# Kernel optimization log

Measured on AMD Instinct MI355X. Metric: run time of the kernel, lower is better.

Reference implementation:

```python
import jax, jax.numpy as jnp
import numpy as np

NUM_HEADS = 16


def setup_inputs() -> dict:
    key = jax.random.key(0)
    ks = jax.random.split(key, 6)
    B, N, M, D = 4, 2048, 2048, 1024
    s = 1.0 / np.sqrt(D)
    return {
        "inputs": jax.random.normal(ks[0], (B, N, D), dtype=jnp.float32),
        "encoderOutputs": jax.random.normal(ks[1], (B, M, D), dtype=jnp.float32),
        "wq": jax.random.normal(ks[2], (D, D), dtype=jnp.float32) * s,
        "wk": jax.random.normal(ks[3], (D, D), dtype=jnp.float32) * s,
        "wv": jax.random.normal(ks[4], (D, D), dtype=jnp.float32) * s,
        "wo": jax.random.normal(ks[5], (D, D), dtype=jnp.float32) * s,
    }


def reference(inputs, encoderOutputs, wq, wk, wv, wo):
    B, N, D = inputs.shape
    M = encoderOutputs.shape[1]
    H = NUM_HEADS
    hd = D // H
    # Linear layers (no bias; torch Linear computes x @ W.T, weights here stored as [dOut,dIn])
    q = (inputs @ wq.T).reshape(B, N, H, hd).transpose(0, 2, 1, 3)        # [B,H,N,hd]
    k = (encoderOutputs @ wk.T).reshape(B, M, H, hd).transpose(0, 2, 1, 3)  # [B,H,M,hd]
    v = (encoderOutputs @ wv.T).reshape(B, M, H, hd).transpose(0, 2, 1, 3)  # [B,H,M,hd]
    scores = jnp.einsum('bhnd,bhmd->bhnm', q, k) / jnp.sqrt(jnp.float32(hd))
    attn = jax.nn.softmax(scores, axis=-1)  # dropout p=0.0 -> identity
    ctx = jnp.einsum('bhnm,bhmd->bhnd', attn, v)
    ctx = ctx.transpose(0, 2, 1, 3).reshape(B, N, D)
    return ctx @ wo.T
```

## Files before the change

kernel.cpp:

```cpp
#include <hip/hip_runtime.h>
#include <hip/hip_bf16.h>


typedef __attribute__((ext_vector_type(8))) short bf16x8;
typedef __attribute__((ext_vector_type(4))) float f32x4;
typedef __attribute__((ext_vector_type(16))) float f32x16;
typedef __attribute__((ext_vector_type(4))) unsigned short u16x4;
typedef __attribute__((ext_vector_type(4))) unsigned int u32x4;

#define SEQ 2048
#define H_ 16

static __device__ __forceinline__ unsigned short f2bf(float f) {
  unsigned int u = __float_as_uint(f);
  u += 0x7fffu + ((u >> 16) & 1u);
  return (unsigned short)(u >> 16);
}

static __device__ __forceinline__ void gload16(const void* g, void* l) {
  __builtin_amdgcn_global_load_lds((const __attribute__((address_space(1))) void*)g,
                                   (__attribute__((address_space(3))) void*)l, 16, 0, 0);
}

__global__ __launch_bounds__(256) void k_cvt_all(const float* __restrict__ x, const float* __restrict__ e,
    const float* __restrict__ wq, const float* __restrict__ wk,
    const float* __restrict__ wv, const float* __restrict__ wo,
    unsigned short* __restrict__ Xb, unsigned short* __restrict__ Eb,
    unsigned short* __restrict__ Wqb, unsigned short* __restrict__ Wkb,
    unsigned short* __restrict__ Wvb, unsigned short* __restrict__ Wob) {
  int i = blockIdx.x * 256 + threadIdx.x;
  const float* src; unsigned short* dst; int off;
  if (i < 2097152)      { src = x;  dst = Xb;  off = i; }
  else if (i < 4194304) { src = e;  dst = Eb;  off = i - 2097152; }
  else if (i < 4456448) { src = wq; dst = Wqb; off = i - 4194304; }
  else if (i < 4718592) { src = wk; dst = Wkb; off = i - 4456448; }
  else if (i < 4980736) { src = wv; dst = Wvb; off = i - 4718592; }
  else                  { src = wo; dst = Wob; off = i - 4980736; }
  float4 v = reinterpret_cast<const float4*>(src)[off];
  u16x4 o;
  o[0] = f2bf(v.x); o[1] = f2bf(v.y); o[2] = f2bf(v.z); o[3] = f2bf(v.w);
  *reinterpret_cast<u16x4*>(dst + (size_t)off * 4) = o;
}

template<typename EPI>
static __device__ __forceinline__ void gemm_core(const unsigned short* __restrict__ A,
                                                 const unsigned short* __restrict__ W,
                                                 int col0, int row0, EPI epi) {
  __shared__ __align__(16) unsigned short As[128 * 32];
  __shared__ __align__(16) unsigned short Bs[128 * 32];
  const int tid = threadIdx.x, lane = tid & 63, w = tid >> 6;
  const int wr = w >> 1, wc = w & 1;
  f32x4 acc[4][4];
  for (int i = 0; i < 4; ++i)
    for (int j = 0; j < 4; ++j)
      for (int e = 0; e < 4; ++e) acc[i][j][e] = 0.f;
  const unsigned short* Ag[2];
  const unsigned short* Wg[2];
  unsigned short* Al[2];
  unsigned short* Bl[2];
  for (int p = 0; p < 2; ++p) {
    int ci = p * 4 + w;
    int eo = ci * 512 + lane * 8;
    int r = eo >> 5, c = eo & 31;
    Ag[p] = A + (size_t)(row0 + r) * 1024 + c;
    Wg[p] = W + (size_t)(col0 + r) * 1024 + c;
    Al[p] = &As[ci * 512];
    Bl[p] = &Bs[ci * 512];
  }
  const int fr = lane & 15, ko = (lane >> 4) * 8;
  for (int k0 = 0; k0 < 1024; k0 += 32) {
    __syncthreads();
    for (int p = 0; p < 2; ++p) {
      gload16(Ag[p] + k0, Al[p]);
      gload16(Wg[p] + k0, Bl[p]);
    }
    __syncthreads();
    bf16x8 af[4], bfr[4];
    for (int mi = 0; mi < 4; ++mi)
      af[mi] = *(const bf16x8*)&As[(wr * 64 + mi * 16 + fr) * 32 + ko];
    for (int ni = 0; ni < 4; ++ni)
      bfr[ni] = *(const bf16x8*)&Bs[(wc * 64 + ni * 16 + fr) * 32 + ko];
    for (int mi = 0; mi < 4; ++mi)
      for (int ni = 0; ni < 4; ++ni)
        acc[mi][ni] = __builtin_amdgcn_mfma_f32_16x16x32_bf16(af[mi], bfr[ni], acc[mi][ni], 0, 0, 0);
  }
  for (int mi = 0; mi < 4; ++mi)
    for (int ni = 0; ni < 4; ++ni) {
      int r0 = row0 + wr * 64 + mi * 16 + (lane >> 4) * 4;
      int o = col0 + wc * 64 + ni * 16 + (lane & 15);
      epi(r0, o, acc[mi][ni]);
    }
}

__global__ __launch_bounds__(256) void k_gemm_qkv(const unsigned short* __restrict__ Xb,
                                                  const unsigned short* __restrict__ Eb,
                                                  const unsigned short* __restrict__ Wqb,
                                                  const unsigned short* __restrict__ Wkb,
                                                  const unsigned short* __restrict__ Wvb,
                                                  unsigned short* __restrict__ Qb,
                                                  unsigned short* __restrict__ Kb,
                                                  unsigned short* __restrict__ Vtg) {
  const int z = blockIdx.z;
  const int col0 = blockIdx.x * 128, row0 = blockIdx.y * 128;
  const unsigned short* A = (z == 0) ? Xb : Eb;
  const unsigned short* W = (z == 0) ? Wqb : (z == 1) ? Wkb : Wvb;
  if (z == 2) {
    gemm_core(A, W, col0, row0, [&](int r0, int o, f32x4 v) {
      int b = r0 >> 11, n0 = r0 & (SEQ - 1);
      int h = o >> 6, c = o & 63;
      u16x4 o4;
      for (int j = 0; j < 4; ++j) o4[j] = f2bf(v[j]);
      *(u16x4*)&Vtg[(((size_t)(b * H_ + h)) * 64 + c) * SEQ + n0] = o4;
    });
  } else {
    unsigned short* out = (z == 0) ? Qb : Kb;
    const float sc = (z == 0) ? 0.18033688f : 1.0f;
    gemm_core(A, W, col0, row0, [&](int r0, int o, f32x4 v) {
      int b = r0 >> 11, n0 = r0 & (SEQ - 1);
      int h = o >> 6, c = o & 63;
      for (int j = 0; j < 4; ++j)
        out[(((size_t)(b * H_ + h)) * SEQ + n0 + j) * 64 + c] = f2bf(v[j] * sc);
    });
  }
}

__global__ __launch_bounds__(256) void k_gemm_out(const unsigned short* __restrict__ A,
                                                  const unsigned short* __restrict__ W,
                                                  float* __restrict__ out) {
  const int col0 = blockIdx.x * 128, row0 = blockIdx.y * 128;
  gemm_core(A, W, col0, row0, [&](int r0, int o, f32x4 v) {
    for (int j = 0; j < 4; ++j)
      out[(size_t)(r0 + j) * 1024 + o] = v[j];
  });
}

static __device__ __forceinline__ int swzaddr(int row, int colb) {
  return row * 128 + (colb ^ ((row & 7) << 4));
}

__global__ __launch_bounds__(512) void k_attn(const unsigned short* __restrict__ Qh,
                                              const unsigned short* __restrict__ Kh,
                                              const unsigned short* __restrict__ Vtg,
                                              unsigned short* __restrict__ CTX) {
  __shared__ __align__(16) char lds[4 * 8192];
  const int tid = threadIdx.x, lane = tid & 63, w = tid >> 6;
  const int hi = lane >> 5, q = lane & 31;
  const int id = blockIdx.x;
  const int bh = (id & 7) * 8 + ((id >> 3) & 7);
  const int qt = id >> 6;
  const size_t kvbase = (size_t)bh * (SEQ * 64);
  const size_t qrow = (size_t)bh * SEQ + qt * 256 + w * 32 + q;
  bf16x8 qf[4];
#pragma unroll
  for (int c = 0; c < 4; ++c)
    qf[c] = *(const bf16x8*)&Qh[qrow * 64 + c * 16 + hi * 8];
  f32x16 oacc0, oacc1, oaccL, fzero;
#pragma unroll
  for (int r = 0; r < 16; ++r) { oacc0[r] = 0.f; oacc1[r] = 0.f; oaccL[r] = 0.f; fzero[r] = 0.f; }
  bf16x8 ones;
#pragma unroll
  for (int r = 0; r < 8; ++r) ones[r] = (short)0x3F80;

  const int sc = tid;
  const int srow = sc >> 3, spb = (sc & 7) << 4;
  const int sge = (spb ^ ((srow & 7) << 4)) >> 1;
  const size_t koff = (size_t)srow * 64 + sge;
  const size_t voff = (size_t)srow * SEQ + sge;
  const int ldso = sc * 16;

#define STAGE(T, BUFO)                                                        \
  {                                                                           \
    gload16(Kh + kvbase + (size_t)(T) * 4096 + koff, lds + (BUFO) + ldso);    \
    gload16(Vtg + kvbase + (size_t)(T) * 64 + voff, lds + (BUFO) + 8192 + ldso); \
  }

  STAGE(0, 0);

  for (int t = 0; t < 32; ++t) {
    __syncthreads();
    const int bo = (t & 1) * 16384;
    char* Kb = lds + bo;
    char* Vb = lds + bo + 8192;
    if (t + 1 < 32) STAGE(t + 1, ((t + 1) & 1) * 16384);

    f32x16 s0, s1;
    __builtin_amdgcn_s_setprio(1);
    {
      bf16x8 kf0 = *(const bf16x8*)(Kb + swzaddr(q, 0 * 32 + hi * 16));
      bf16x8 kf1 = *(const bf16x8*)(Kb + swzaddr(32 + q, 0 * 32 + hi * 16));
      s0 = __builtin_amdgcn_mfma_f32_32x32x16_bf16(kf0, qf[0], fzero, 0, 0, 0);
      s1 = __builtin_amdgcn_mfma_f32_32x32x16_bf16(kf1, qf[0], fzero, 0, 0, 0);
    }
#pragma unroll
    for (int c = 1; c < 4; ++c) {
      bf16x8 kf0 = *(const bf16x8*)(Kb + swzaddr(q, c * 32 + hi * 16));
      bf16x8 kf1 = *(const bf16x8*)(Kb + swzaddr(32 + q, c * 32 + hi * 16));
      s0 = __builtin_amdgcn_mfma_f32_32x32x16_bf16(kf0, qf[c], s0, 0, 0, 0);
      s1 = __builtin_amdgcn_mfma_f32_32x32x16_bf16(kf1, qf[c], s1, 0, 0, 0);
    }
    __builtin_amdgcn_s_setprio(0);

    bf16x8 pfrag[4];

#define SOFT_PACK(SREG, FA, FB)                                               \
    {                                                                         \
      float pa[16];                                                           \
      _Pragma("unroll")                                                       \
      for (int r = 0; r < 16; ++r) pa[r] = __builtin_amdgcn_exp2f(SREG[r]);   \
      unsigned pw[8];                                                         \
      _Pragma("unroll")                                                       \
      for (int i = 0; i < 8; ++i)                                             \
        asm("v_cvt_pk_bf16_f32 %0, %1, %2" : "=v"(pw[i])                      \
            : "v"(pa[2 * i]), "v"(pa[2 * i + 1]));                            \
      asm("v_permlane32_swap_b32 %0, %1" : "+v"(pw[0]), "+v"(pw[2]));         \
      asm("v_permlane32_swap_b32 %0, %1" : "+v"(pw[1]), "+v"(pw[3]));         \
      asm("v_permlane32_swap_b32 %0, %1" : "+v"(pw[4]), "+v"(pw[6]));         \
      asm("v_permlane32_swap_b32 %0, %1" : "+v"(pw[5]), "+v"(pw[7]));         \
      u32x4 fa = { pw[0], pw[1], pw[2], pw[3] };                              \
      u32x4 fb = { pw[4], pw[5], pw[6], pw[7] };                              \
      FA = __builtin_bit_cast(bf16x8, fa);                                    \
      FB = __builtin_bit_cast(bf16x8, fb);                                    \
    }

    SOFT_PACK(s0, pfrag[0], pfrag[1])
    SOFT_PACK(s1, pfrag[2], pfrag[3])
#undef SOFT_PACK

    __builtin_amdgcn_s_setprio(1);
#pragma unroll
    for (int kk = 0; kk < 4; ++kk) {
      bf16x8 vf0 = *(const bf16x8*)(Vb + swzaddr(q, kk * 32 + hi * 16));
      bf16x8 vf1 = *(const bf16x8*)(Vb + swzaddr(32 + q, kk * 32 + hi * 16));
      oacc0 = __builtin_amdgcn_mfma_f32_32x32x16_bf16(vf0, pfrag[kk], oacc0, 0, 0, 0);
      oacc1 = __builtin_amdgcn_mfma_f32_32x32x16_bf16(vf1, pfrag[kk], oacc1, 0, 0, 0);
      oaccL = __builtin_amdgcn_mfma_f32_32x32x16_bf16(ones, pfrag[kk], oaccL, 0, 0, 0);
    }
    __builtin_amdgcn_s_setprio(0);
  }
#undef STAGE

  const float inv = 1.0f / oaccL[0];
  const int b = bh >> 4, h = bh & 15;
  const size_t orow = ((size_t)b * SEQ + qt * 256 + w * 32 + q) * 1024 + h * 64;
#pragma unroll
  for (int g = 0; g < 4; ++g) {
    u16x4 o0, o1;
#pragma unroll
    for (int j = 0; j < 4; ++j) {
      o0[j] = f2bf(oacc0[g * 4 + j] * inv);
      o1[j] = f2bf(oacc1[g * 4 + j] * inv);
    }
    *(u16x4*)&CTX[orow + g * 8 + hi * 4] = o0;
    *(u16x4*)&CTX[orow + 32 + g * 8 + hi * 4] = o1;
  }
}

extern "C" void kernel_launch(void* const* d_in, const int* in_sizes, int n_in,
                              void* d_out, int out_size, void* d_ws, size_t ws_size,
                              hipStream_t stream) {
  const float* x  = (const float*)d_in[0];
  const float* e  = (const float*)d_in[1];
  const float* wq = (const float*)d_in[2];
  const float* wk = (const float*)d_in[3];
  const float* wv = (const float*)d_in[4];
  const float* wo = (const float*)d_in[5];
  unsigned short* Xb  = (unsigned short*)d_ws;
  unsigned short* Eb  = Xb + 8388608;
  unsigned short* Wqb = Eb + 8388608;
  unsigned short* Wkb = Wqb + 1048576;
  unsigned short* Wvb = Wkb + 1048576;
  unsigned short* Wob = Wvb + 1048576;
  unsigned short* Qb  = Wob + 1048576;
  unsigned short* Kb  = Qb + 8388608;
  unsigned short* Vtg = Kb + 8388608;
  unsigned short* Cb  = Vtg + 8388608;

  k_cvt_all<<<20480, 256, 0, stream>>>(x, e, wq, wk, wv, wo, Xb, Eb, Wqb, Wkb, Wvb, Wob);

  k_gemm_qkv<<<dim3(8, 64, 3), 256, 0, stream>>>(Xb, Eb, Wqb, Wkb, Wvb, Qb, Kb, Vtg);

  k_attn<<<512, 512, 0, stream>>>(Qb, Kb, Vtg, Cb);

  k_gemm_out<<<dim3(8, 64), 256, 0, stream>>>(Cb, Wob, (float*)d_out);
}
```

Before: 206.9 us.

## Fuse fp32-to-bf16 activation conversion into QKV GEMM tile loads

The separate conversion pass no longer writes bf16 copies of the inputs and encoder outputs. The QKV GEMM now loads fp32 activation tiles straight into LDS with an XOR swizzle and converts them to bf16 in registers with v_cvt_pk_bf16_f32 before the MFMAs. This removes a full read-write pass over the 32MB of activations and one extra round trip through memory. In exchange the GEMM A-tile traffic doubles (fp32 instead of bf16), the A LDS buffer grows, and conversion work is repeated by every column block that reuses the same A tile.

```diff
diff --git a/kernel.cpp b/kernel.cpp
--- a/kernel.cpp
+++ b/kernel.cpp
@@ -22,65 +22,113 @@
                                    (__attribute__((address_space(3))) void*)l, 16, 0, 0);
 }
 
-__global__ __launch_bounds__(256) void k_cvt_all(const float* __restrict__ x, const float* __restrict__ e,
-    const float* __restrict__ wq, const float* __restrict__ wk,
+__global__ __launch_bounds__(256) void k_cvt_w(const float* __restrict__ wq, const float* __restrict__ wk,
     const float* __restrict__ wv, const float* __restrict__ wo,
-    unsigned short* __restrict__ Xb, unsigned short* __restrict__ Eb,
     unsigned short* __restrict__ Wqb, unsigned short* __restrict__ Wkb,
     unsigned short* __restrict__ Wvb, unsigned short* __restrict__ Wob) {
   int i = blockIdx.x * 256 + threadIdx.x;
   const float* src; unsigned short* dst; int off;
-  if (i < 2097152)      { src = x;  dst = Xb;  off = i; }
-  else if (i < 4194304) { src = e;  dst = Eb;  off = i - 2097152; }
-  else if (i < 4456448) { src = wq; dst = Wqb; off = i - 4194304; }
-  else if (i < 4718592) { src = wk; dst = Wkb; off = i - 4456448; }
-  else if (i < 4980736) { src = wv; dst = Wvb; off = i - 4718592; }
-  else                  { src = wo; dst = Wob; off = i - 4980736; }
+  if (i < 262144)       { src = wq; dst = Wqb; off = i; }
+  else if (i < 524288)  { src = wk; dst = Wkb; off = i - 262144; }
+  else if (i < 786432)  { src = wv; dst = Wvb; off = i - 524288; }
+  else                  { src = wo; dst = Wob; off = i - 786432; }
   float4 v = reinterpret_cast<const float4*>(src)[off];
   u16x4 o;
   o[0] = f2bf(v.x); o[1] = f2bf(v.y); o[2] = f2bf(v.z); o[3] = f2bf(v.w);
   *reinterpret_cast<u16x4*>(dst + (size_t)off * 4) = o;
 }
 
-template<typename EPI>
-static __device__ __forceinline__ void gemm_core(const unsigned short* __restrict__ A,
+template<int F32A, typename EPI>
+static __device__ __forceinline__ void gemm_core(const void* __restrict__ Av,
                                                  const unsigned short* __restrict__ W,
                                                  int col0, int row0, EPI epi) {
-  __shared__ __align__(16) unsigned short As[128 * 32];
-  __shared__ __align__(16) unsigned short Bs[128 * 32];
+  constexpr int ABYTES = F32A ? 16384 : 8192;
+  __shared__ __align__(16) char AsB[ABYTES];
+  __shared__ __align__(16) unsigned short Ws[128 * 32];
   const int tid = threadIdx.x, lane = tid & 63, w = tid >> 6;
   const int wr = w >> 1, wc = w & 1;
   f32x4 acc[4][4];
   for (int i = 0; i < 4; ++i)
     for (int j = 0; j < 4; ++j)
       for (int e = 0; e < 4; ++e) acc[i][j][e] = 0.f;
-  const unsigned short* Ag[2];
-  const unsigned short* Wg[2];
-  unsigned short* Al[2];
-  unsigned short* Bl[2];
-  for (int p = 0; p < 2; ++p) {
-    int ci = p * 4 + w;
-    int eo = ci * 512 + lane * 8;
-    int r = eo >> 5, c = eo & 31;
-    Ag[p] = A + (size_t)(row0 + r) * 1024 + c;
-    Wg[p] = W + (size_t)(col0 + r) * 1024 + c;
-    Al[p] = &As[ci * 512];
-    Bl[p] = &Bs[ci * 512];
-  }
+
+  size_t aoff[F32A ? 4 : 2];
+  int aldso[F32A ? 4 : 2];
+  if (F32A) {
+    const float* Af = (const float*)Av;
+    (void)Af;
+#pragma unroll
+    for (int h = 0; h < 4; ++h) {
+      int ch = tid + h * 256;
+      int row = ch >> 3, colb = (ch & 7) << 4;
+      int ge = (colb ^ ((row & 7) << 4)) >> 2;
+      aoff[h] = (size_t)(row0 + row) * 1024 + ge;
+      aldso[h] = ch * 16;
+    }
+  } else {
+#pragma unroll
+    for (int h = 0; h < 2; ++h) {
+      int ch = tid + h * 256;
+      int row = ch >> 2, c8 = (ch & 3) * 8;
+      aoff[h] = (size_t)(row0 + row) * 1024 + c8;
+      aldso[h] = ch * 16;
+    }
+  }
+  size_t woff[2];
+  int wldso[2];
+#pragma unroll
+  for (int h = 0; h < 2; ++h) {
+    int ch = tid + h * 256;
+    int row = ch >> 2, c8 = (ch & 3) * 8;
+    woff[h] = (size_t)(col0 + row) * 1024 + c8;
+    wldso[h] = ch * 16;
+  }
+
   const int fr = lane & 15, ko = (lane >> 4) * 8;
   for (int k0 = 0; k0 < 1024; k0 += 32) {
     __syncthreads();
-    for (int p = 0; p < 2; ++p) {
-      gload16(Ag[p] + k0, Al[p]);
-      gload16(Wg[p] + k0, Bl[p]);
-    }
+    if (F32A) {
+      const float* Af = (const float*)Av;
+#pragma unroll
+      for (int h = 0; h < 4; ++h)
+        gload16(Af + aoff[h] + k0, AsB + aldso[h]);
+    } else {
+      const unsigned short* Ab = (const unsigned short*)Av;
+#pragma unroll
+      for (int h = 0; h < 2; ++h)
+        gload16(Ab + aoff[h] + k0, AsB + aldso[h]);
+    }
+#pragma unroll
+    for (int h = 0; h < 2; ++h)
+      gload16(W + woff[h] + k0, (char*)Ws + wldso[h]);
     __syncthreads();
+
     bf16x8 af[4], bfr[4];
+#pragma unroll
+    for (int mi = 0; mi < 4; ++mi) {
+      int r = wr * 64 + mi * 16 + fr;
+      if (F32A) {
+        int swz = (r & 7) << 4;
+        int b0 = r * 128 + ko * 4;
+        f32x4 x0 = *(const f32x4*)(AsB + ((b0) ^ swz));
+        f32x4 x1 = *(const f32x4*)(AsB + ((b0 + 16) ^ swz));
+        unsigned pw[4];
+        asm("v_cvt_pk_bf16_f32 %0, %1, %2" : "=v"(pw[0]) : "v"(x0[0]), "v"(x0[1]));
+        asm("v_cvt_pk_bf16_f32 %0, %1, %2" : "=v"(pw[1]) : "v"(x0[2]), "v"(x0[3]));
+        asm("v_cvt_pk_bf16_f32 %0, %1, %2" : "=v"(pw[2]) : "v"(x1[0]), "v"(x1[1]));
+        asm("v_cvt_pk_bf16_f32 %0, %1, %2" : "=v"(pw[3]) : "v"(x1[2]), "v"(x1[3]));
+        u32x4 fa = { pw[0], pw[1], pw[2], pw[3] };
+        af[mi] = __builtin_bit_cast(bf16x8, fa);
+      } else {
+        af[mi] = *(const bf16x8*)(AsB + (r * 32 + ko) * 2);
+      }
+    }
+#pragma unroll
+    for (int ni = 0; ni < 4; ++ni)
+      bfr[ni] = *(const bf16x8*)&Ws[(wc * 64 + ni * 16 + fr) * 32 + ko];
+#pragma unroll
     for (int mi = 0; mi < 4; ++mi)
-      af[mi] = *(const bf16x8*)&As[(wr * 64 + mi * 16 + fr) * 32 + ko];
-    for (int ni = 0; ni < 4; ++ni)
-      bfr[ni] = *(const bf16x8*)&Bs[(wc * 64 + ni * 16 + fr) * 32 + ko];
-    for (int mi = 0; mi < 4; ++mi)
+#pragma unroll
       for (int ni = 0; ni < 4; ++ni)
         acc[mi][ni] = __builtin_amdgcn_mfma_f32_16x16x32_bf16(af[mi], bfr[ni], acc[mi][ni], 0, 0, 0);
   }
@@ -92,8 +140,8 @@
     }
 }
 
-__global__ __launch_bounds__(256) void k_gemm_qkv(const unsigned short* __restrict__ Xb,
-                                                  const unsigned short* __restrict__ Eb,
+__global__ __launch_bounds__(256) void k_gemm_qkv(const float* __restrict__ x,
+                                                  const float* __restrict__ e,
                                                   const unsigned short* __restrict__ Wqb,
                                                   const unsigned short* __restrict__ Wkb,
                                                   const unsigned short* __restrict__ Wvb,
@@ -102,10 +150,10 @@
                                                   unsigned short* __restrict__ Vtg) {
   const int z = blockIdx.z;
   const int col0 = blockIdx.x * 128, row0 = blockIdx.y * 128;
-  const unsigned short* A = (z == 0) ? Xb : Eb;
+  const void* A = (z == 0) ? (const void*)x : (const void*)e;
   const unsigned short* W = (z == 0) ? Wqb : (z == 1) ? Wkb : Wvb;
   if (z == 2) {
-    gemm_core(A, W, col0, row0, [&](int r0, int o, f32x4 v) {
+    gemm_core<1>(A, W, col0, row0, [&](int r0, int o, f32x4 v) {
       int b = r0 >> 11, n0 = r0 & (SEQ - 1);
       int h = o >> 6, c = o & 63;
       u16x4 o4;
@@ -115,7 +163,7 @@
   } else {
     unsigned short* out = (z == 0) ? Qb : Kb;
     const float sc = (z == 0) ? 0.18033688f : 1.0f;
-    gemm_core(A, W, col0, row0, [&](int r0, int o, f32x4 v) {
+    gemm_core<1>(A, W, col0, row0, [&](int r0, int o, f32x4 v) {
       int b = r0 >> 11, n0 = r0 & (SEQ - 1);
       int h = o >> 6, c = o & 63;
       for (int j = 0; j < 4; ++j)
@@ -128,7 +176,7 @@
                                                   const unsigned short* __restrict__ W,
                                                   float* __restrict__ out) {
   const int col0 = blockIdx.x * 128, row0 = blockIdx.y * 128;
-  gemm_core(A, W, col0, row0, [&](int r0, int o, f32x4 v) {
+  gemm_core<0>(A, W, col0, row0, [&](int r0, int o, f32x4 v) {
     for (int j = 0; j < 4; ++j)
       out[(size_t)(r0 + j) * 1024 + o] = v[j];
   });
@@ -264,9 +312,7 @@
   const float* wk = (const float*)d_in[3];
   const float* wv = (const float*)d_in[4];
   const float* wo = (const float*)d_in[5];
-  unsigned short* Xb  = (unsigned short*)d_ws;
-  unsigned short* Eb  = Xb + 8388608;
-  unsigned short* Wqb = Eb + 8388608;
+  unsigned short* Wqb = (unsigned short*)d_ws;
   unsigned short* Wkb = Wqb + 1048576;
   unsigned short* Wvb = Wkb + 1048576;
   unsigned short* Wob = Wvb + 1048576;
@@ -275,9 +321,9 @@
   unsigned short* Vtg = Kb + 8388608;
   unsigned short* Cb  = Vtg + 8388608;
 
-  k_cvt_all<<<20480, 256, 0, stream>>>(x, e, wq, wk, wv, wo, Xb, Eb, Wqb, Wkb, Wvb, Wob);
-
-  k_gemm_qkv<<<dim3(8, 64, 3), 256, 0, stream>>>(Xb, Eb, Wqb, Wkb, Wvb, Qb, Kb, Vtg);
+  k_cvt_w<<<4096, 256, 0, stream>>>(wq, wk, wv, wo, Wqb, Wkb, Wvb, Wob);
+
+  k_gemm_qkv<<<dim3(8, 64, 3), 256, 0, stream>>>(x, e, Wqb, Wkb, Wvb, Qb, Kb, Vtg);
 
   k_attn<<<512, 512, 0, stream>>>(Qb, Kb, Vtg, Cb);
 
```

Result: slower. 239.6 us (+15.8%).
